# Kernel optimization log

Hardware: AMD Instinct MI355X
Metric: run time of the kernel (lower is better)

The kernel has to match this reference:

```python
import jax, jax.numpy as jnp
import numpy as np

N_RAYS = 32768
N_OBJ = 16
N_SAMPLES = 32   # n_pts_object
N_BASE = 64      # pre-existing coarse samples per ray
MISS = 1e10      # sentinel for non-intersecting slots (sorts to the end)


def _make_transforms(key):
    """Random rigid+scale world-to-object transforms, pytorch3d row-vector convention:
    p' = p @ M[:3,:3] + M[3,:3]."""
    k1, k2, k3 = jax.random.split(key, 3)
    A = jax.random.normal(k1, (N_OBJ, 3, 3))
    Q, _ = jnp.linalg.qr(A)                                   # orthonormal 3x3
    t = jax.random.normal(k2, (N_OBJ, 3)) * 5.0               # translations
    s = jax.random.uniform(k3, (N_OBJ, 3), minval=0.5, maxval=2.0)
    eye = jnp.tile(jnp.eye(4, dtype=jnp.float32), (N_OBJ, 1, 1))
    rots = eye.at[:, :3, :3].set(Q.astype(jnp.float32))
    trafos = rots.at[:, 3, :3].set(t)
    scales = eye.at[:, 0, 0].set(s[:, 0]).at[:, 1, 1].set(s[:, 1]).at[:, 2, 2].set(s[:, 2])
    return trafos, rots, scales


def setup_inputs() -> dict:
    key = jax.random.key(0)
    k0, k1, k2, k3 = jax.random.split(key, 4)
    origins = jax.random.normal(k0, (N_RAYS, 3), dtype=jnp.float32) * 2.0
    directions = jax.random.normal(k1, (N_RAYS, 3), dtype=jnp.float32)
    lengths = jnp.sort(jax.random.uniform(k2, (N_RAYS, N_BASE), dtype=jnp.float32,
                                          minval=0.1, maxval=20.0), axis=-1)
    trafos, rots, scales = _make_transforms(k3)
    return {"origins": origins, "directions": directions, "lengths": lengths,
            "trafos_w2o": trafos, "rots_w2o": rots, "scales_w2o": scales}


def reference(origins, directions, lengths, trafos_w2o, rots_w2o, scales_w2o):
    N = origins.shape[0]
    M = trafos_w2o.shape[0]
    S = N_SAMPLES

    d_w = directions / jnp.linalg.norm(directions, axis=-1, keepdims=True)

    # compose transforms (row-vector convention: compose(m1, m2) -> m1 @ m2)
    pt_mat = trafos_w2o @ scales_w2o     # points world->object, [M,4,4]
    dir_mat = rots_w2o @ scales_w2o      # directions world->object

    # rays in each object frame: [M,N,3]
    origins_o = jnp.einsum('ni,mij->mnj', origins, pt_mat[:, :3, :3]) + pt_mat[:, None, 3, :3]
    dirs_o = jnp.einsum('ni,mij->mnj', d_w, dir_mat[:, :3, :3])
    dirs_o = dirs_o / jnp.linalg.norm(dirs_o, axis=-1, keepdims=True)

    # slab ray-AABB intersection against unit box [-1,1]^3
    inv = 1.0 / dirs_o
    t0 = (-1.0 - origins_o) * inv
    t1 = (1.0 - origins_o) * inv
    tmin = jnp.max(jnp.minimum(t0, t1), axis=-1)   # [M,N]
    tmax = jnp.min(jnp.maximum(t0, t1), axis=-1)
    hit = (tmax > tmin) & (tmax > 0.0)
    t_in = jnp.maximum(tmin, 0.0)

    # BoxRaysampler: linspace between entry and exit
    lin = jnp.linspace(0.0, 1.0, S, dtype=origins.dtype)
    z_o = t_in[..., None] + (tmax - t_in)[..., None] * lin          # [M,N,S]

    # object-space sample points / dirs
    pts_o = origins_o[:, :, None] + dirs_o[:, :, None] * z_o[..., None]   # [M,N,S,3]
    dirs_o_s = jnp.broadcast_to(dirs_o[:, :, None], pts_o.shape)

    # back to world -> z along world ray
    o2w = jnp.linalg.inv(pt_mat)
    pts_w = jnp.einsum('mnsi,mij->mnsj', pts_o, o2w[:, :3, :3]) + o2w[:, None, None, 3, :3]
    z_w = jnp.einsum('mnsj,nj->mns', pts_w - origins[None, :, None], d_w)
    z_w = jnp.where(hit[..., None], z_w, MISS)                      # mask misses

    # scatter into per-ray lengths (static worst-case size), then sort per ray
    z_flat = jnp.transpose(z_w, (1, 0, 2)).reshape(N, M * S)        # [N, M*S]
    lengths_new = jnp.concatenate([lengths, z_flat], axis=-1)       # [N, B+M*S]

    node_ids = jnp.broadcast_to(jnp.arange(M, dtype=jnp.int32)[:, None, None], (M, N, S))
    node_ids = jnp.where(hit[..., None], node_ids, -1)
    node_flat = jnp.concatenate(
        [jnp.full((N, lengths.shape[-1]), -1, dtype=jnp.int32),
         jnp.transpose(node_ids, (1, 0, 2)).reshape(N, M * S)], axis=-1)
    mask_flat = jnp.concatenate(
        [jnp.zeros((N, lengths.shape[-1]), dtype=bool),
         jnp.transpose(jnp.broadcast_to(hit[..., None], (M, N, S)), (1, 0, 2)).reshape(N, M * S)],
        axis=-1)

    order = jnp.argsort(lengths_new, axis=-1)
    sorted_lengths = jnp.take_along_axis(lengths_new, order, axis=-1)
    sorted_nodes = jnp.take_along_axis(node_flat, order, axis=-1)
    sorted_mask = jnp.take_along_axis(mask_flat, order, axis=-1)

    # flattened object-space samples (zeroed for misses; static shape)
    pts_flat = (pts_o * hit[..., None, None]).reshape(-1, 3)
    dirs_flat = (dirs_o_s * hit[..., None, None]).reshape(-1, 3)

    return sorted_lengths, sorted_nodes, sorted_mask, pts_flat, dirs_flat
```

## Files before the change

kernel.cpp:

```cpp
#include <hip/hip_runtime.h>

#define NR    32768
#define NOBJ  16
#define NS    32
#define NB    64
#define WIDTH 576
#define MISSV 1e10f

__device__ __forceinline__ float fmulr(float a, float b){ return __fmul_rn(a,b); }
__device__ __forceinline__ float faddr(float a, float b){ return __fadd_rn(a,b); }
__device__ __forceinline__ float fsubr(float a, float b){ return __fsub_rn(a,b); }
__device__ __forceinline__ float fdvr (float a, float b){ return __fdiv_rn(a,b); }

struct RayObj {
  float oo[3];
  float dd[3];
  float t_in, dt;
  float dn;
  bool  hit;
};

__device__ __forceinline__ void ray_obj_setup(
    const float* __restrict__ origins, const float* __restrict__ dirs,
    const float* __restrict__ trafos,  const float* __restrict__ scales,
    int m, int n, RayObj& R)
{
  const float o0 = origins[3*n+0], o1 = origins[3*n+1], o2 = origins[3*n+2];
  const float r0 = dirs[3*n+0],    r1 = dirs[3*n+1],    r2 = dirs[3*n+2];
  const float nn = __fsqrt_rn(faddr(faddr(fmulr(r0,r0), fmulr(r1,r1)), fmulr(r2,r2)));
  const float w0 = fdvr(r0,nn), w1 = fdvr(r1,nn), w2 = fdvr(r2,nn);

  const float* T = trafos + 16*m;
  const float* S = scales + 16*m;
  const float s0 = S[0], s1 = S[5], s2 = S[10];
  const float pm00 = fmulr(T[0],  s0), pm01 = fmulr(T[1],  s1), pm02 = fmulr(T[2],  s2);
  const float pm10 = fmulr(T[4],  s0), pm11 = fmulr(T[5],  s1), pm12 = fmulr(T[6],  s2);
  const float pm20 = fmulr(T[8],  s0), pm21 = fmulr(T[9],  s1), pm22 = fmulr(T[10], s2);
  const float tm0  = fmulr(T[12], s0), tm1  = fmulr(T[13], s1), tm2  = fmulr(T[14], s2);

  const float oo0 = faddr(faddr(faddr(fmulr(o0,pm00), fmulr(o1,pm10)), fmulr(o2,pm20)), tm0);
  const float oo1 = faddr(faddr(faddr(fmulr(o0,pm01), fmulr(o1,pm11)), fmulr(o2,pm21)), tm1);
  const float oo2 = faddr(faddr(faddr(fmulr(o0,pm02), fmulr(o1,pm12)), fmulr(o2,pm22)), tm2);
  const float du0 = faddr(faddr(fmulr(w0,pm00), fmulr(w1,pm10)), fmulr(w2,pm20));
  const float du1 = faddr(faddr(fmulr(w0,pm01), fmulr(w1,pm11)), fmulr(w2,pm21));
  const float du2 = faddr(faddr(fmulr(w0,pm02), fmulr(w1,pm12)), fmulr(w2,pm22));
  const float dn  = __fsqrt_rn(faddr(faddr(fmulr(du0,du0), fmulr(du1,du1)), fmulr(du2,du2)));
  const float dd0 = fdvr(du0,dn), dd1 = fdvr(du1,dn), dd2 = fdvr(du2,dn);

  const float i0 = fdvr(1.0f, dd0), i1 = fdvr(1.0f, dd1), i2 = fdvr(1.0f, dd2);
  const float a0 = fmulr(fsubr(-1.0f, oo0), i0), b0 = fmulr(fsubr(1.0f, oo0), i0);
  const float a1 = fmulr(fsubr(-1.0f, oo1), i1), b1 = fmulr(fsubr(1.0f, oo1), i1);
  const float a2 = fmulr(fsubr(-1.0f, oo2), i2), b2 = fmulr(fsubr(1.0f, oo2), i2);
  const float tmn = fmaxf(fmaxf(fminf(a0,b0), fminf(a1,b1)), fminf(a2,b2));
  const float tmx = fminf(fminf(fmaxf(a0,b0), fmaxf(a1,b1)), fmaxf(a2,b2));

  R.hit  = (tmx > tmn) && (tmx > 0.0f);
  R.t_in = fmaxf(tmn, 0.0f);
  R.dt   = fsubr(tmx, R.t_in);
  R.dn   = dn;
  R.oo[0]=oo0; R.oo[1]=oo1; R.oo[2]=oo2;
  R.dd[0]=dd0; R.dd[1]=dd1; R.dd[2]=dd2;
}

__device__ __forceinline__ int count_run(const float* __restrict__ K,
                                         const float* __restrict__ A,
                                         const float* __restrict__ B,
                                         const float* __restrict__ IB,
                                         int m2, float key, bool tie)
{
  const float A2 = A[m2], B2 = B[m2];
  const float* V = K + NB + m2 * NS;
  if (B2 <= 0.0f) {
    return (A2 < key || (A2 == key && tie)) ? NS : 0;
  }
  float g = floorf(fmulr(fsubr(key, A2), IB[m2]));
  g = fminf(33.0f, fmaxf(-1.0f, g));
  int c = (int)g + 1;
  c = c < 0 ? 0 : (c > NS ? NS : c);
  while (c > 0)  { const float v = V[c-1]; if (v < key || (v == key && tie)) break; --c; }
  while (c < NS) { const float v = V[c];   if (v < key || (v == key && tie)) ++c; else break; }
  return c;
}

struct PtsS  { float ld[64][8]; };
struct SortS {
  float sKeys[4][WIDTH];
  float sA[4][NOBJ], sB[4][NOBJ], sIB[4][NOBJ];
  float sL[4][WIDTH], sN[4][WIDTH];
};
union __align__(16) Smem { PtsS p; SortS s; };

__global__ __launch_bounds__(256) void k_fused(
    const float* __restrict__ origins, const float* __restrict__ dirs,
    const float* __restrict__ lengths,
    const float* __restrict__ trafos,  const float* __restrict__ scales,
    float* __restrict__ outL, float* __restrict__ outN, float* __restrict__ outM,
    float* __restrict__ outP, float* __restrict__ outD)
{
  __shared__ Smem U;
  const int tid  = threadIdx.x;
  const int role = blockIdx.x & 1;
  const int bid  = blockIdx.x >> 1;

  if (role == 0) {
    const int m   = bid >> 9;
    const int n0  = (bid & 511) << 6;
    if (tid < 64) {
      RayObj R;
      ray_obj_setup(origins, dirs, trafos, scales, m, n0 + tid, R);
      const bool h = R.hit;
      U.p.ld[tid][0] = h ? R.oo[0] : 0.0f;
      U.p.ld[tid][1] = h ? R.oo[1] : 0.0f;
      U.p.ld[tid][2] = h ? R.oo[2] : 0.0f;
      U.p.ld[tid][3] = h ? R.dd[0] : 0.0f;
      U.p.ld[tid][4] = h ? R.dd[1] : 0.0f;
      U.p.ld[tid][5] = h ? R.t_in  : 0.0f;
      U.p.ld[tid][6] = h ? R.dt    : 0.0f;
      U.p.ld[tid][7] = h ? R.dd[2] : 0.0f;
    }
    __syncthreads();
    const size_t base = (size_t)(m * NR + n0) * 96;
    float4* P4 = (float4*)(outP + base);
    float4* D4 = (float4*)(outD + base);
    #pragma unroll
    for (int it = 0; it < 6; ++it) {
      const int f   = tid + (it << 8);
      const int rr  = f / 24;
      const int off = (f - rr * 24) * 4;
      const float oox = U.p.ld[rr][0], ooy = U.p.ld[rr][1], ooz = U.p.ld[rr][2];
      const float ddx = U.p.ld[rr][3], ddy = U.p.ld[rr][4], ddz = U.p.ld[rr][7];
      const float ti  = U.p.ld[rr][5], dtt = U.p.ld[rr][6];
      float4 p, d;
      float* pp = (float*)&p; float* dv = (float*)&d;
      #pragma unroll
      for (int i = 0; i < 4; ++i) {
        const int idx = off + i;
        const int s   = idx / 3;
        const int c   = idx - s * 3;
        const float z  = ti + dtt * ((float)s * (1.0f/31.0f));
        const float oc = (c == 0) ? oox : ((c == 1) ? ooy : ooz);
        const float dc = (c == 0) ? ddx : ((c == 1) ? ddy : ddz);
        pp[i] = oc + dc * z;
        dv[i] = dc;
      }
      P4[f] = p;
      D4[f] = d;
    }
    return;
  }

  const int wv   = tid >> 6;
  const int lane = tid & 63;
  const int n    = bid * 4 + wv;

  if (lane < NOBJ) {
    RayObj R;
    ray_obj_setup(origins, dirs, trafos, scales, lane, n, R);
    float myA = MISSV, myB = -1.0f, myIB = 0.0f;
    if (R.hit) {
      const double invdn = 1.0 / (double)R.dn;
      myA = (float)((double)R.t_in * invdn);
      myB = (float)(((double)R.dt * invdn) * (1.0 / 31.0));
      if (!(myB > 0.0f)) myB = 0.0f;
      myIB = (myB > 0.0f) ? (1.0f / myB) : 0.0f;
    }
    U.s.sA[wv][lane]  = myA;
    U.s.sB[wv][lane]  = R.hit ? myB : -1.0f;
    U.s.sIB[wv][lane] = myIB;
  }
  __syncthreads();

  unsigned hm = 0;
  #pragma unroll
  for (int mm = 0; mm < NOBJ; ++mm) hm |= (U.s.sB[wv][mm] >= 0.0f ? 1u : 0u) << mm;
  const int H = __popc(hm);

  float kr[9];
  kr[0] = lengths[n * NB + lane];
  U.s.sKeys[wv][lane] = kr[0];
  #pragma unroll
  for (int k = 1; k < 9; ++k) {
    const int m0 = 2*(k-1) + (lane >> 5);
    const int s  = lane & 31;
    const float A_ = U.s.sA[wv][m0], B_ = U.s.sB[wv][m0];
    const float key = (B_ < 0.0f) ? MISSV : faddr(A_, fmulr(B_, (float)s));
    kr[k] = key;
    U.s.sKeys[wv][64*k + lane] = key;
  }
  __syncthreads();

  const float* K = U.s.sKeys[wv];
  #pragma unroll
  for (int k = 0; k < 9; ++k) {
    const float key = kr[k];
    int rank; float nodef; float outkey = key;
    if (k == 0) {
      rank = lane;
      unsigned mm = hm;
      while (mm) { const int m2 = __ffs(mm) - 1; mm &= mm - 1;
        rank += count_run(K, U.s.sA[wv], U.s.sB[wv], U.s.sIB[wv], m2, key, false); }
      nodef = -1.0f;
    } else {
      const int m = 2*(k-1) + (lane >> 5);
      const int s = lane & 31;
      if (!((hm >> m) & 1u)) {
        const int MB = __popc((~hm) & ((1u << m) - 1u) & 0xFFFFu);
        rank  = NB + NS*H + NS*MB + s;
        nodef = -1.0f; outkey = MISSV;
      } else {
        rank = s;
        int c = 0;
        #pragma unroll
        for (int st = 64; st >= 1; st >>= 1) {
          const int t2 = c + st;
          if (t2 <= NB && K[t2-1] <= key) c = t2;
        }
        rank += c;
        unsigned mm = hm & ~(1u << m);
        while (mm) { const int m2 = __ffs(mm) - 1; mm &= mm - 1;
          rank += count_run(K, U.s.sA[wv], U.s.sB[wv], U.s.sIB[wv], m2, key, m2 < m); }
        nodef = (float)m;
      }
    }
    U.s.sL[wv][rank] = outkey;
    U.s.sN[wv][rank] = nodef;
  }
  __syncthreads();

  float4* pL = (float4*)(outL + (size_t)n * WIDTH);
  float4* pN = (float4*)(outN + (size_t)n * WIDTH);
  float4* pM = (float4*)(outM + (size_t)n * WIDTH);
  const float4* qL = (const float4*)U.s.sL[wv];
  const float4* qN = (const float4*)U.s.sN[wv];
  for (int i = lane; i < WIDTH/4; i += 64) pL[i] = qL[i];
  for (int i = lane; i < WIDTH/4; i += 64) {
    const float4 nv = qN[i];
    float4 mv;
    mv.x = nv.x >= 0.0f ? 1.0f : 0.0f;
    mv.y = nv.y >= 0.0f ? 1.0f : 0.0f;
    mv.z = nv.z >= 0.0f ? 1.0f : 0.0f;
    mv.w = nv.w >= 0.0f ? 1.0f : 0.0f;
    pN[i] = nv;
    pM[i] = mv;
  }
}

extern "C" void kernel_launch(void* const* d_in, const int* in_sizes, int n_in,
                              void* d_out, int out_size, void* d_ws, size_t ws_size,
                              hipStream_t stream)
{
  (void)in_sizes; (void)n_in; (void)out_size; (void)d_ws; (void)ws_size;
  const float* origins = (const float*)d_in[0];
  const float* dirs    = (const float*)d_in[1];
  const float* lengths = (const float*)d_in[2];
  const float* trafos  = (const float*)d_in[3];
  const float* scales  = (const float*)d_in[5];

  float* out  = (float*)d_out;
  float* outL = out;
  float* outN = out + (size_t)NR * WIDTH;
  float* outM = out + (size_t)2 * NR * WIDTH;
  float* outP = out + (size_t)3 * NR * WIDTH;
  float* outD = outP + (size_t)NOBJ * NR * NS * 3;

  hipLaunchKernelGGL(k_fused, dim3(16384), dim3(256), 0, stream,
                     origins, dirs, lengths, trafos, scales,
                     outL, outN, outM, outP, outD);
}
```

Baseline: 622.2 us.

## Drop block barriers in sort path and recompute run keys in registers

```diff
diff --git a/kernel.cpp b/kernel.cpp
--- a/kernel.cpp
+++ b/kernel.cpp
@@ -62,29 +62,31 @@
   R.dd[0]=dd0; R.dd[1]=dd1; R.dd[2]=dd2;
 }
 
-__device__ __forceinline__ int count_run(const float* __restrict__ K,
-                                         const float* __restrict__ A,
-                                         const float* __restrict__ B,
-                                         const float* __restrict__ IB,
-                                         int m2, float key, bool tie)
-{
-  const float A2 = A[m2], B2 = B[m2];
-  const float* V = K + NB + m2 * NS;
+__device__ __forceinline__ int count_run_reg(float A2, float B2, float IB2,
+                                             float key, bool tie)
+{
   if (B2 <= 0.0f) {
     return (A2 < key || (A2 == key && tie)) ? NS : 0;
   }
-  float g = floorf(fmulr(fsubr(key, A2), IB[m2]));
+  float g = floorf(fmulr(fsubr(key, A2), IB2));
   g = fminf(33.0f, fmaxf(-1.0f, g));
   int c = (int)g + 1;
   c = c < 0 ? 0 : (c > NS ? NS : c);
-  while (c > 0)  { const float v = V[c-1]; if (v < key || (v == key && tie)) break; --c; }
-  while (c < NS) { const float v = V[c];   if (v < key || (v == key && tie)) ++c; else break; }
+  while (c > 0) {
+    const float v = faddr(A2, fmulr(B2, (float)(c-1)));
+    if (v < key || (v == key && tie)) break;
+    --c;
+  }
+  while (c < NS) {
+    const float v = faddr(A2, fmulr(B2, (float)c));
+    if (v < key || (v == key && tie)) ++c; else break;
+  }
   return c;
 }
 
 struct PtsS  { float ld[64][8]; };
 struct SortS {
-  float sKeys[4][WIDTH];
+  float sBase[4][NB];
   float sA[4][NOBJ], sB[4][NOBJ], sIB[4][NOBJ];
   float sL[4][WIDTH], sN[4][WIDTH];
 };
@@ -153,9 +155,11 @@
   const int lane = tid & 63;
   const int n    = bid * 4 + wv;
 
+  bool myhit = false;
   if (lane < NOBJ) {
     RayObj R;
     ray_obj_setup(origins, dirs, trafos, scales, lane, n, R);
+    myhit = R.hit;
     float myA = MISSV, myB = -1.0f, myIB = 0.0f;
     if (R.hit) {
       const double invdn = 1.0 / (double)R.dn;
@@ -168,64 +172,73 @@
     U.s.sB[wv][lane]  = R.hit ? myB : -1.0f;
     U.s.sIB[wv][lane] = myIB;
   }
-  __syncthreads();
-
-  unsigned hm = 0;
-  #pragma unroll
-  for (int mm = 0; mm < NOBJ; ++mm) hm |= (U.s.sB[wv][mm] >= 0.0f ? 1u : 0u) << mm;
+  const unsigned hm = (unsigned)(__ballot(myhit) & 0xFFFFull);
   const int H = __popc(hm);
+  asm volatile("" ::: "memory");
 
   float kr[9];
   kr[0] = lengths[n * NB + lane];
-  U.s.sKeys[wv][lane] = kr[0];
+  U.s.sBase[wv][lane] = kr[0];
   #pragma unroll
   for (int k = 1; k < 9; ++k) {
     const int m0 = 2*(k-1) + (lane >> 5);
     const int s  = lane & 31;
-    const float A_ = U.s.sA[wv][m0], B_ = U.s.sB[wv][m0];
-    const float key = (B_ < 0.0f) ? MISSV : faddr(A_, fmulr(B_, (float)s));
-    kr[k] = key;
-    U.s.sKeys[wv][64*k + lane] = key;
-  }
-  __syncthreads();
-
-  const float* K = U.s.sKeys[wv];
+    if ((hm >> m0) & 1u) {
+      const float A_ = U.s.sA[wv][m0], B_ = U.s.sB[wv][m0];
+      kr[k] = faddr(A_, fmulr(B_, (float)s));
+    } else {
+      kr[k] = MISSV;
+    }
+  }
+  asm volatile("" ::: "memory");
+
+  const float* K = U.s.sBase[wv];
+  int rnk[9];
+  rnk[0] = lane;
   #pragma unroll
-  for (int k = 0; k < 9; ++k) {
-    const float key = kr[k];
-    int rank; float nodef; float outkey = key;
-    if (k == 0) {
-      rank = lane;
-      unsigned mm = hm;
-      while (mm) { const int m2 = __ffs(mm) - 1; mm &= mm - 1;
-        rank += count_run(K, U.s.sA[wv], U.s.sB[wv], U.s.sIB[wv], m2, key, false); }
-      nodef = -1.0f;
+  for (int k = 1; k < 9; ++k) {
+    const int m = 2*(k-1) + (lane >> 5);
+    const int s = lane & 31;
+    if ((hm >> m) & 1u) {
+      int c = 0;
+      const float key = kr[k];
+      #pragma unroll
+      for (int st = 64; st >= 1; st >>= 1) {
+        const int t2 = c + st;
+        if (t2 <= NB && K[t2-1] <= key) c = t2;
+      }
+      rnk[k] = s + c;
     } else {
+      const int MB = __popc((~hm) & ((1u << m) - 1u) & 0xFFFFu);
+      rnk[k] = NB + NS*H + NS*MB + s;
+    }
+  }
+
+  unsigned mm = hm;
+  while (mm) {
+    const int m2 = __ffs(mm) - 1; mm &= mm - 1;
+    const float A2  = U.s.sA[wv][m2];
+    const float B2  = U.s.sB[wv][m2];
+    const float IB2 = U.s.sIB[wv][m2];
+    rnk[0] += count_run_reg(A2, B2, IB2, kr[0], false);
+    #pragma unroll
+    for (int k = 1; k < 9; ++k) {
       const int m = 2*(k-1) + (lane >> 5);
-      const int s = lane & 31;
-      if (!((hm >> m) & 1u)) {
-        const int MB = __popc((~hm) & ((1u << m) - 1u) & 0xFFFFu);
-        rank  = NB + NS*H + NS*MB + s;
-        nodef = -1.0f; outkey = MISSV;
-      } else {
-        rank = s;
-        int c = 0;
-        #pragma unroll
-        for (int st = 64; st >= 1; st >>= 1) {
-          const int t2 = c + st;
-          if (t2 <= NB && K[t2-1] <= key) c = t2;
-        }
-        rank += c;
-        unsigned mm = hm & ~(1u << m);
-        while (mm) { const int m2 = __ffs(mm) - 1; mm &= mm - 1;
-          rank += count_run(K, U.s.sA[wv], U.s.sB[wv], U.s.sIB[wv], m2, key, m2 < m); }
-        nodef = (float)m;
-      }
-    }
-    U.s.sL[wv][rank] = outkey;
-    U.s.sN[wv][rank] = nodef;
-  }
-  __syncthreads();
+      if (((hm >> m) & 1u) && m != m2)
+        rnk[k] += count_run_reg(A2, B2, IB2, kr[k], m2 < m);
+    }
+  }
+
+  U.s.sL[wv][rnk[0]] = kr[0];
+  U.s.sN[wv][rnk[0]] = -1.0f;
+  #pragma unroll
+  for (int k = 1; k < 9; ++k) {
+    const int m = 2*(k-1) + (lane >> 5);
+    const bool h = (hm >> m) & 1u;
+    U.s.sL[wv][rnk[k]] = kr[k];
+    U.s.sN[wv][rnk[k]] = h ? (float)m : -1.0f;
+  }
+  asm volatile("" ::: "memory");
 
   float4* pL = (float4*)(outL + (size_t)n * WIDTH);
   float4* pN = (float4*)(outN + (size_t)n * WIDTH);
```

Result: no change. 622.7 us (+0.1%).
